# Performance work log

Hardware: AMD Instinct MI355X
Metric: run time of the kernel (lower is better)

The kernel has to match this reference:

```python
import jax, jax.numpy as jnp
import numpy as np
from jax import lax

B, C, H, W = 16, 384, 28, 28
HEADS = 8


def _ln(x, g, b):
    mu = jnp.mean(x, axis=-1, keepdims=True)
    var = jnp.var(x, axis=-1, keepdims=True)
    return (x - mu) * lax.rsqrt(var + 1e-5) * g + b


def setup_inputs() -> dict:
    key = jax.random.key(0)
    ks = jax.random.split(key, 8)
    s = 0.02
    return {
        "cls_token": jax.random.normal(ks[0], (B, 1, C), dtype=jnp.float32),
        "x": jax.random.normal(ks[1], (B, C, H, W), dtype=jnp.float32),
        "conv_w": jax.random.normal(ks[2], (C, 1, 3, 3), dtype=jnp.float32) * s,
        "conv_b": jnp.zeros((C,), jnp.float32),
        "ln1_g": jnp.ones((C,), jnp.float32),
        "ln1_b": jnp.zeros((C,), jnp.float32),
        "qkv_w": jax.random.normal(ks[3], (3 * C, C), dtype=jnp.float32) * s,
        "proj_w": jax.random.normal(ks[4], (C, C), dtype=jnp.float32) * s,
        "proj_b": jnp.zeros((C,), jnp.float32),
        "ln2_g": jnp.ones((C,), jnp.float32),
        "ln2_b": jnp.zeros((C,), jnp.float32),
        "fc1_w": jax.random.normal(ks[5], (4 * C, C), dtype=jnp.float32) * s,
        "fc1_b": jnp.zeros((4 * C,), jnp.float32),
        "fc2_w": jax.random.normal(ks[6], (C, 4 * C), dtype=jnp.float32) * s,
        "fc2_b": jnp.zeros((C,), jnp.float32),
    }


def reference(cls_token, x, conv_w, conv_b, ln1_g, ln1_b, qkv_w, proj_w, proj_b,
              ln2_g, ln2_b, fc1_w, fc1_b, fc2_w, fc2_b):
    Bv, Cv, Hv, Wv = x.shape
    h = HEADS
    d = Cv // h
    # depthwise 3x3 positional conv (groups=dim), residual add
    pe = lax.conv_general_dilated(
        x, conv_w, window_strides=(1, 1), padding="SAME",
        feature_group_count=Cv,
        dimension_numbers=("NCHW", "OIHW", "NCHW")) + conv_b[None, :, None, None]
    x = x + pe
    x_patch = x.reshape(Bv, Cv, Hv * Wv).transpose(0, 2, 1)  # [B, HW, C]
    xc = jnp.concatenate([cls_token, x_patch], axis=1)       # [B, N, C]
    N = xc.shape[1]

    # --- Attention with inline global_attn stats (first-call / int sentinel path) ---
    y = _ln(xc, ln1_g, ln1_b)
    qkv = (y @ qkv_w.T).reshape(Bv, N, 3, h, d)
    q = qkv[:, :, 0].transpose(0, 2, 1, 3)  # [B, h, N, d]
    k = qkv[:, :, 1].transpose(0, 2, 1, 3)
    v = qkv[:, :, 2].transpose(0, 2, 1, 3)
    scale = d ** -0.5
    attn = jax.nn.softmax(jnp.einsum("bhnd,bhmd->bhnm", q, k) * scale, axis=-1)
    # per-token global attention statistic: mean over heads of cls row (excl. cls)
    global_attn = jnp.mean(attn[:, :, 0, 1:], axis=1)  # [B, N-1]
    o = jnp.einsum("bhnm,bhmd->bhnd", attn, v).transpose(0, 2, 1, 3).reshape(Bv, N, Cv)
    xc = xc + (o @ proj_w.T + proj_b)

    # --- MLP (GELU exact, matching torch nn.GELU default) ---
    y2 = _ln(xc, ln2_g, ln2_b)
    m = jax.nn.gelu(y2 @ fc1_w.T + fc1_b, approximate=False) @ fc2_w.T + fc2_b
    xc = xc + m

    cls_out = xc[:, :1]                                            # [B, 1, C]
    x_out = xc[:, 1:].transpose(0, 2, 1).reshape(Bv, Cv, Hv, Wv)    # [B, C, H, W]
    return cls_out, x_out, global_attn
```

## Files before the change

### kernel.cpp

```cpp
#include <hip/hip_runtime.h>
#include <hip/hip_bf16.h>

#define DI __device__ __forceinline__

typedef __attribute__((ext_vector_type(4))) float f32x4;
typedef __attribute__((ext_vector_type(8))) short bf16x8;
typedef __attribute__((ext_vector_type(4))) short bf16x4;

static constexpr int CB = 16;
static constexpr int CC = 384;
static constexpr int CH = 28, CW = 28;
static constexpr int CD = 48;
static constexpr int CN = 785;
static constexpr int CM = CB * CN;
static constexpr int C3 = 3 * CC;
static constexpr int CF = 4 * CC;
static constexpr int HW = CH * CW;
static constexpr int NP = 832;

DI short f2b(float f) {
  __hip_bfloat16 h = __float2bfloat16(f);
  return *reinterpret_cast<short*>(&h);
}
DI float b2f(short s) {
  union { unsigned u; float f; } x;
  x.u = ((unsigned)(unsigned short)s) << 16;
  return x.f;
}

DI void gload16(const short* g, short* l) {
  __builtin_amdgcn_global_load_lds((const __attribute__((address_space(1))) void*)g,
                                   (__attribute__((address_space(3))) void*)l, 16, 0, 0);
}

__global__ void k_misc(const float* __restrict__ cls, float* __restrict__ xc,
                       float* __restrict__ ga) {
  const int gid = blockIdx.x * 256 + threadIdx.x;
  if (gid < CB * HW) ga[gid] = 0.f;
  if (gid < CB * CC) {
    const int b = gid / CC, c = gid % CC;
    xc[((size_t)b * CN) * CC + c] = cls[gid];
  }
}

__global__ void k_wconv(const float* __restrict__ s0, const float* __restrict__ s1,
                        const float* __restrict__ s2, const float* __restrict__ s3,
                        short* __restrict__ dst) {
  const int gid = (blockIdx.x * 256 + threadIdx.x) * 4;
  if (gid >= 1769472) return;
  const float* s; int off;
  if (gid < 442368)       { s = s0; off = gid; }
  else if (gid < 589824)  { s = s1; off = gid - 442368; }
  else if (gid < 1179648) { s = s2; off = gid - 589824; }
  else                    { s = s3; off = gid - 1179648; }
  f32x4 v = *(const f32x4*)(s + off);
  bf16x4 o;
#pragma unroll
  for (int i = 0; i < 4; i++) o[i] = f2b(v[i]);
  *(bf16x4*)(dst + gid) = o;
}

__global__ __launch_bounds__(256) void k_conv_t(const float* __restrict__ x,
                                                const float* __restrict__ cw,
                                                const float* __restrict__ cb,
                                                float* __restrict__ xc) {
  __shared__ float T[64][65];
  __shared__ float Wc[64 * 9];
  __shared__ float Cbs[64];
  const int b = blockIdx.z;
  const int cc = blockIdx.y * 64;
  const int hw0 = blockIdx.x * 64;
  const int t = threadIdx.x;
  const int hwi = t & 63, ci0 = t >> 6;
  const int hw = hw0 + hwi;
  const int yy = hw / CW, xx = hw % CW;
  const int ci2 = t & 63, hb2 = t >> 6;

  for (int i = t; i < 64 * 9; i += 256) Wc[i] = cw[cc * 9 + i];
  if (t < 64) Cbs[t] = cb[cc + t];
  __syncthreads();
  if (hw < HW) {
    const int ctr = yy * CW + xx;
    int off9[9]; float mk9[9];
#pragma unroll
    for (int ky = 0; ky < 3; ky++)
#pragma unroll
      for (int kx = 0; kx < 3; kx++) {
        const int iy = yy + ky - 1, ix = xx + kx - 1;
        const bool v = (iy >= 0 && iy < CH && ix >= 0 && ix < CW);
        off9[ky * 3 + kx] = v ? iy * CW + ix : ctr;
        mk9[ky * 3 + kx] = v ? 1.f : 0.f;
      }
#pragma unroll
    for (int j = 0; j < 16; j += 2) {
      const int cl0 = ci0 * 16 + j;
      const float* xp0 = x + ((size_t)(b * CC + cc + cl0)) * HW;
      const float* xp1 = xp0 + HW;
      float t0[9], t1[9];
#pragma unroll
      for (int q = 0; q < 9; q++) { t0[q] = xp0[off9[q]]; t1[q] = xp1[off9[q]]; }
      const float c0 = xp0[ctr], c1 = xp1[ctr];
      float a0 = Cbs[cl0], a1 = Cbs[cl0 + 1];
#pragma unroll
      for (int q = 0; q < 9; q++) {
        a0 += Wc[cl0 * 9 + q] * (t0[q] * mk9[q]);
        a1 += Wc[(cl0 + 1) * 9 + q] * (t1[q] * mk9[q]);
      }
      T[cl0][hwi] = c0 + a0;
      T[cl0 + 1][hwi] = c1 + a1;
    }
  }
  __syncthreads();
#pragma unroll
  for (int j = 0; j < 16; j++) {
    const int hwl = hb2 + j * 4;
    if (hw0 + hwl < HW)
      xc[((size_t)b * CN + 1 + hw0 + hwl) * CC + cc + ci2] = T[ci2][hwl];
  }
}

__global__ __launch_bounds__(256) void k_ln(const float* __restrict__ xin,
                                            const float* __restrict__ g,
                                            const float* __restrict__ bta,
                                            short* __restrict__ y, int Mtot) {
  const int row = blockIdx.x * 4 + (threadIdx.x >> 6);
  const int l = threadIdx.x & 63;
  if (row >= Mtot) return;
  const float* xr = xin + (size_t)row * CC;
  float v[6], s = 0.f, ss = 0.f;
#pragma unroll
  for (int i = 0; i < 6; i++) {
    v[i] = xr[l + i * 64];
    s += v[i];
    ss += v[i] * v[i];
  }
#pragma unroll
  for (int m = 1; m < 64; m <<= 1) { s += __shfl_xor(s, m); ss += __shfl_xor(ss, m); }
  const float mu = s * (1.f / CC);
  const float var = ss * (1.f / CC) - mu * mu;
  const float r = rsqrtf(var + 1e-5f);
#pragma unroll
  for (int i = 0; i < 6; i++) {
    const int c = l + i * 64;
    y[(size_t)row * CC + c] = f2b((v[i] - mu) * r * g[c] + bta[c]);
  }
}

template <int BM, int DOGELU, int DORES, int DOBIAS, int OUTBF>
__global__ __launch_bounds__(256) void k_gemm(const short* __restrict__ A,
                                              const short* __restrict__ W,
                                              const float* __restrict__ bias,
                                              const float* __restrict__ resid,
                                              void* __restrict__ out_,
                                              int M, int N, int K, int NN) {
  constexpr int MI = BM / 32;
  constexpr int ACALLS = BM / 64;
  constexpr int ASZ = BM * 32, BSZ = 128 * 32;
  __shared__ short As[2 * ASZ];
  __shared__ short Bs[2 * BSZ];

  const int nwg = gridDim.x;
  const int q = nwg >> 3, r = nwg & 7;
  const int x = blockIdx.x & 7, j = blockIdx.x >> 3;
  const int base = (x < r) ? x * (q + 1) : r * (q + 1) + (x - r) * q;
  const int wgid = base + j;
  const int bm = (wgid / NN) * BM, bn = (wgid % NN) * 128;

  const int t = threadIdx.x, w = t >> 6, l = t & 63, g = l >> 4, li = l & 15;
  const int wm = (w >> 1) * (BM / 2), wn = (w & 1) * 64;

  const int srow = l >> 2;
  const int scol = (l & 3) * 8;
  const short* aSrc[ACALLS]; int aOff[ACALLS];
#pragma unroll
  for (int jj = 0; jj < ACALLS; jj++) {
    int arow = bm + w * (BM / 4) + jj * 16 + srow; if (arow > M - 1) arow = M - 1;
    aSrc[jj] = A + (size_t)arow * K + scol;
    aOff[jj] = (w * (BM / 4) + jj * 16) * 32;
  }
  const short* bSrc[2]; int bOff[2];
#pragma unroll
  for (int jj = 0; jj < 2; jj++) {
    const int brow = bn + w * 32 + jj * 16 + srow;
    bSrc[jj] = W + (size_t)brow * K + scol;
    bOff[jj] = (w * 32 + jj * 16) * 32;
  }

  auto stage = [&](int buf, int kt) {
    const int ko = kt * 32;
#pragma unroll
    for (int jj = 0; jj < ACALLS; jj++)
      gload16(aSrc[jj] + ko, &As[buf * ASZ] + aOff[jj]);
#pragma unroll
    for (int jj = 0; jj < 2; jj++)
      gload16(bSrc[jj] + ko, &Bs[buf * BSZ] + bOff[jj]);
  };

  f32x4 acc[MI][4] = {};
  const int nkt = K / 32;
  stage(0, 0);
  __syncthreads();
  int cur = 0;
  for (int kt = 0; kt < nkt; kt++) {
    if (kt + 1 < nkt) stage(cur ^ 1, kt + 1);
    const short* Ab = &As[cur * ASZ];
    const short* Bb = &Bs[cur * BSZ];
    bf16x8 af[MI], bf[4];
#pragma unroll
    for (int mi = 0; mi < MI; mi++)
      af[mi] = *(const bf16x8*)&Ab[(wm + mi * 16 + li) * 32 + g * 8];
#pragma unroll
    for (int ni = 0; ni < 4; ni++)
      bf[ni] = *(const bf16x8*)&Bb[(wn + ni * 16 + li) * 32 + g * 8];
#pragma unroll
    for (int mi = 0; mi < MI; mi++)
#pragma unroll
      for (int ni = 0; ni < 4; ni++)
        acc[mi][ni] = __builtin_amdgcn_mfma_f32_16x16x32_bf16(af[mi], bf[ni], acc[mi][ni], 0, 0, 0);
    __syncthreads();
    cur ^= 1;
  }

#pragma unroll
  for (int mi = 0; mi < MI; mi++)
#pragma unroll
    for (int ni = 0; ni < 4; ni++) {
      const int col = bn + wn + ni * 16 + li;
      float bv = 0.f;
      if constexpr (DOBIAS) bv = bias[col];
#pragma unroll
      for (int rr = 0; rr < 4; rr++) {
        const int row = bm + wm + mi * 16 + g * 4 + rr;
        if (row < M) {
          float v = acc[mi][ni][rr] + bv;
          if constexpr (DOGELU) v = 0.5f * v * (1.f + erff(v * 0.7071067811865475f));
          if constexpr (DORES) v += resid[(size_t)row * N + col];
          if constexpr (OUTBF)
            ((short*)out_)[(size_t)row * N + col] = f2b(v);
          else
            ((float*)out_)[(size_t)row * N + col] = v;
        }
      }
    }
}

__global__ __launch_bounds__(256) void k_vt(const short* __restrict__ qkv,
                                            short* __restrict__ vt) {
  __shared__ short Tl[48 * 71];
  const int n0 = blockIdx.x * 64;
  const int bh = blockIdx.y;
  const int b = bh >> 3, h = bh & 7;
  const int t = threadIdx.x;
  const size_t bbase = (size_t)b * CN;
#pragma unroll
  for (int it = 0; it < 2; it++) {
    const int gi = t + it * 256;
    if (gi < 384) {
      const int nrel = gi / 6, dg = gi % 6;
      const int n = n0 + nrel;
      bf16x8 val = {};
      if (n < CN)
        val = *(const bf16x8*)(qkv + (bbase + n) * C3 + 2 * CC + h * CD + dg * 8);
#pragma unroll
      for (int i = 0; i < 8; i++) Tl[(dg * 8 + i) * 71 + nrel] = val[i];
    }
  }
  __syncthreads();
#pragma unroll
  for (int it = 0; it < 2; it++) {
    const int gj = t + it * 256;
    if (gj < 384) {
      const int d = gj >> 3, ng = gj & 7;
      bf16x8 v;
#pragma unroll
      for (int i = 0; i < 8; i++) v[i] = Tl[d * 71 + ng * 8 + i];
      *(bf16x8*)(vt + ((size_t)bh * CD + d) * NP + n0 + ng * 8) = v;
    }
  }
}

__global__ __launch_bounds__(256) void k_attn(const short* __restrict__ qkv,
                                              const short* __restrict__ vt,
                                              short* __restrict__ o) {
  __shared__ short Ks[64 * 48];
  __shared__ short Vs[48 * 64];
  const int f = blockIdx.x;
  const int xslot = f & 7, grp = f >> 3;
  const int bh = xslot + 8 * (grp & 15);
  const int qt = grp >> 4;
  const int b = bh >> 3, h = bh & 7;
  const int q0 = qt * 64;
  const int t = threadIdx.x, w = t >> 6, l = t & 63, g = l >> 4, li = l & 15;
  const size_t bbase = (size_t)b * CN;

  const int qrow = q0 + w * 16 + li;
  const int qr = qrow > CN - 1 ? CN - 1 : qrow;
  const short* qb = qkv + (bbase + qr) * C3 + h * CD;
  bf16x8 qf0 = *(const bf16x8*)(qb + g * 8);
  bf16x8 qf1 = {};
  if (g < 2) qf1 = *(const bf16x8*)(qb + 32 + g * 8);

  float mr = -1e30f, ls = 0.f;
  f32x4 oa[3] = {};
  const float scale = 0.14433756729740643f;

  const int krow0 = t / 6, kcg0 = t % 6;
  const int krow1 = (t + 256) / 6, kcg1 = (t + 256) % 6;
  const int vd0 = t >> 3, vkvg0 = t & 7;
  const int vd1 = (t + 256) >> 3, vkvg1 = (t + 256) & 7;
  const short* kbase = qkv + bbase * C3 + CC + h * CD;
  const short* vbase = vt + (size_t)bh * CD * NP;

  bf16x8 kr0 = {}, kr1 = {}, vr0 = {}, vr1 = {};
  kr0 = *(const bf16x8*)(kbase + (size_t)min(krow0, CN - 1) * C3 + kcg0 * 8);
  vr0 = *(const bf16x8*)(vbase + vd0 * NP + vkvg0 * 8);
  if (t < 128) {
    kr1 = *(const bf16x8*)(kbase + (size_t)min(krow1, CN - 1) * C3 + kcg1 * 8);
    vr1 = *(const bf16x8*)(vbase + vd1 * NP + vkvg1 * 8);
  }

  for (int kt = 0; kt < 13; kt++) {
    const int kv0 = kt * 64;
    __syncthreads();
    *(bf16x8*)((char*)Ks + ((krow0 * 96 + kcg0 * 16) ^ ((krow0 & 7) << 4))) = kr0;
    *(bf16x8*)((char*)Vs + ((vd0 * 128 + vkvg0 * 16) ^ ((vd0 & 7) << 4))) = vr0;
    if (t < 128) {
      *(bf16x8*)((char*)Ks + ((krow1 * 96 + kcg1 * 16) ^ ((krow1 & 7) << 4))) = kr1;
      *(bf16x8*)((char*)Vs + ((vd1 * 128 + vkvg1 * 16) ^ ((vd1 & 7) << 4))) = vr1;
    }
    __syncthreads();
    if (kt < 12) {
      const int kn = kv0 + 64;
      kr0 = *(const bf16x8*)(kbase + (size_t)min(kn + krow0, CN - 1) * C3 + kcg0 * 8);
      vr0 = *(const bf16x8*)(vbase + vd0 * NP + kn + vkvg0 * 8);
      if (t < 128) {
        kr1 = *(const bf16x8*)(kbase + (size_t)min(kn + krow1, CN - 1) * C3 + kcg1 * 8);
        vr1 = *(const bf16x8*)(vbase + vd1 * NP + kn + vkvg1 * 8);
      }
    }

    f32x4 s[4];
    __builtin_amdgcn_s_setprio(1);
#pragma unroll
    for (int ni = 0; ni < 4; ni++) {
      const int krw = ni * 16 + li;
      const int sw = (krw & 7) << 4;
      bf16x8 kf0 = *(const bf16x8*)((char*)Ks + ((krw * 96 + g * 16) ^ sw));
      bf16x8 kf1 = {};
      if (g < 2) kf1 = *(const bf16x8*)((char*)Ks + ((krw * 96 + 64 + g * 16) ^ sw));
      f32x4 acc = {};
      acc = __builtin_amdgcn_mfma_f32_16x16x32_bf16(kf0, qf0, acc, 0, 0, 0);
      acc = __builtin_amdgcn_mfma_f32_16x16x32_bf16(kf1, qf1, acc, 0, 0, 0);
      s[ni] = acc;
    }
    __builtin_amdgcn_s_setprio(0);

    float mt = -1e30f;
#pragma unroll
    for (int ni = 0; ni < 4; ni++)
#pragma unroll
      for (int rr = 0; rr < 4; rr++) {
        const int kva = kv0 + ni * 16 + g * 4 + rr;
        const float v = (kva < CN) ? s[ni][rr] * scale : -1e30f;
        s[ni][rr] = v;
        mt = fmaxf(mt, v);
      }
    mt = fmaxf(mt, __shfl_xor(mt, 16));
    mt = fmaxf(mt, __shfl_xor(mt, 32));
    const float mn = fmaxf(mr, mt);
    const float al = __expf(mr - mn);
    mr = mn;
    float ps = 0.f;
#pragma unroll
    for (int ni = 0; ni < 4; ni++)
#pragma unroll
      for (int rr = 0; rr < 4; rr++) {
        const float p = __expf(s[ni][rr] - mn);
        s[ni][rr] = p;
        ps += p;
      }
    ps += __shfl_xor(ps, 16);
    ps += __shfl_xor(ps, 32);
    ls = ls * al + ps;

    const int sb = (l & 48) + ((l & 48) >> 2);
    float ar[4];
#pragma unroll
    for (int rr = 0; rr < 4; rr++) ar[rr] = __shfl(al, sb + rr);
#pragma unroll
    for (int d = 0; d < 3; d++)
#pragma unroll
      for (int rr = 0; rr < 4; rr++) oa[d][rr] *= ar[rr];

    bf16x8 pa[2];
#pragma unroll
    for (int ks = 0; ks < 2; ks++)
#pragma unroll
      for (int i = 0; i < 8; i++)
        pa[ks][i] = f2b(i < 4 ? s[2 * ks][i] : s[2 * ks + 1][i - 4]);

    __builtin_amdgcn_s_setprio(1);
#pragma unroll
    for (int d = 0; d < 3; d++) {
      const int drow = d * 16 + li;
      const int sw = (drow & 7) << 4;
#pragma unroll
      for (int ks = 0; ks < 2; ks++) {
        bf16x4 lo = *(const bf16x4*)((char*)Vs + ((drow * 128 + ks * 64 + g * 8) ^ sw));
        bf16x4 hi = *(const bf16x4*)((char*)Vs + ((drow * 128 + ks * 64 + 32 + g * 8) ^ sw));
        bf16x8 vb;
#pragma unroll
        for (int i = 0; i < 4; i++) { vb[i] = lo[i]; vb[4 + i] = hi[i]; }
        oa[d] = __builtin_amdgcn_mfma_f32_16x16x32_bf16(pa[ks], vb, oa[d], 0, 0, 0);
      }
    }
    __builtin_amdgcn_s_setprio(0);
  }

  const int sb = (l & 48) + ((l & 48) >> 2);
  float lr[4];
#pragma unroll
  for (int rr = 0; rr < 4; rr++) lr[rr] = __shfl(ls, sb + rr);
#pragma unroll
  for (int d = 0; d < 3; d++)
#pragma unroll
    for (int rr = 0; rr < 4; rr++) {
      const int n = q0 + w * 16 + g * 4 + rr;
      if (n < CN)
        o[(bbase + n) * CC + h * CD + d * 16 + li] = f2b(oa[d][rr] / lr[rr]);
    }
}

__global__ __launch_bounds__(256) void k_gattn(const short* __restrict__ qkv,
                                               float* __restrict__ ga) {
  const int b = blockIdx.x >> 3, h = blockIdx.x & 7;
  __shared__ float red[4];
  const int t = threadIdx.x;
  const size_t bbase = (size_t)b * CN;
  const short* q0 = qkv + bbase * C3 + h * CD;
  float qv[CD];
#pragma unroll
  for (int i = 0; i < CD; i++) qv[i] = b2f(q0[i]);
  float lg[4], ev[4];
  float lmax = -1e30f;
#pragma unroll
  for (int j = 0; j < 4; j++) {
    const int m = t + j * 256;
    if (m < CN) {
      const short* kr = qkv + (bbase + m) * C3 + CC + h * CD;
      float acc = 0.f;
#pragma unroll
      for (int i = 0; i < CD; i++) acc += qv[i] * b2f(kr[i]);
      lg[j] = acc * 0.14433756729740643f;
      lmax = fmaxf(lmax, lg[j]);
    } else lg[j] = -1e30f;
  }
  for (int msk = 1; msk < 64; msk <<= 1) lmax = fmaxf(lmax, __shfl_xor(lmax, msk));
  if ((t & 63) == 0) red[t >> 6] = lmax;
  __syncthreads();
  lmax = fmaxf(fmaxf(red[0], red[1]), fmaxf(red[2], red[3]));
  __syncthreads();
  float es = 0.f;
#pragma unroll
  for (int j = 0; j < 4; j++) {
    ev[j] = (t + j * 256 < CN) ? __expf(lg[j] - lmax) : 0.f;
    es += ev[j];
  }
  for (int msk = 1; msk < 64; msk <<= 1) es += __shfl_xor(es, msk);
  if ((t & 63) == 0) red[t >> 6] = es;
  __syncthreads();
  es = red[0] + red[1] + red[2] + red[3];
  const float inv = 0.125f / es;
#pragma unroll
  for (int j = 0; j < 4; j++) {
    const int m = t + j * 256;
    if (m >= 1 && m < CN) atomicAdd(&ga[b * HW + m - 1], ev[j] * inv);
  }
}

__global__ __launch_bounds__(256) void k_out(const float* __restrict__ xc,
                                             float* __restrict__ outp) {
  const int b = blockIdx.y, tile = blockIdx.x, t = threadIdx.x;
  if (tile == 78) {
    for (int i = t; i < CC; i += 256)
      outp[b * CC + i] = xc[((size_t)b * CN) * CC + i];
    return;
  }
  __shared__ float T[64][65];
  const int ct = tile / 13, ht = tile % 13;
  const int c0 = ct * 64, hw0 = ht * 64;
  const int ci = t & 63, hb = t >> 6;
  for (int j = 0; j < 16; j++) {
    const int hwl = hb + j * 4;
    if (hw0 + hwl < HW)
      T[ci][hwl] = xc[((size_t)b * CN + 1 + hw0 + hwl) * CC + c0 + ci];
  }
  __syncthreads();
  const int hi = t & 63, cb2 = t >> 6;
  float* xo = outp + CB * CC;
  for (int j = 0; j < 16; j++) {
    const int cl = cb2 + j * 4;
    if (hw0 + hi < HW)
      xo[((size_t)(b * CC + c0 + cl)) * HW + hw0 + hi] = T[cl][hi];
  }
}

extern "C" void kernel_launch(void* const* d_in, const int* in_sizes, int n_in,
                              void* d_out, int out_size, void* d_ws, size_t ws_size,
                              hipStream_t stream) {
  const float* cls    = (const float*)d_in[0];
  const float* x      = (const float*)d_in[1];
  const float* conv_w = (const float*)d_in[2];
  const float* conv_b = (const float*)d_in[3];
  const float* ln1_g  = (const float*)d_in[4];
  const float* ln1_b  = (const float*)d_in[5];
  const float* qkv_w  = (const float*)d_in[6];
  const float* proj_w = (const float*)d_in[7];
  const float* proj_b = (const float*)d_in[8];
  const float* ln2_g  = (const float*)d_in[9];
  const float* ln2_b  = (const float*)d_in[10];
  const float* fc1_w  = (const float*)d_in[11];
  const float* fc1_b  = (const float*)d_in[12];
  const float* fc2_w  = (const float*)d_in[13];
  const float* fc2_b  = (const float*)d_in[14];

  float* outf = (float*)d_out;
  float* ga = outf + (size_t)CB * CC + (size_t)CB * CC * HW;
  short* vtb = (short*)(outf + CB * CC);

  char* ws = (char*)d_ws;
  float* xc   = (float*)ws;
  short* y    = (short*)(ws + 19292160ULL);
  short* qkvb = (short*)(ws + 28938240ULL);
  short* o    = (short*)(ws + 57876480ULL);
  short* m1   = (short*)(ws + 28938240ULL);
  short* wbuf = (short*)(ws + 67522560ULL);
  short* qkv_wb = wbuf;
  short* proj_wb = wbuf + 442368;
  short* fc1_wb  = wbuf + 589824;
  short* fc2_wb  = wbuf + 1179648;

  const int thr = 256;
  k_misc<<<49, thr, 0, stream>>>(cls, xc, ga);
  k_wconv<<<1728, thr, 0, stream>>>(qkv_w, proj_w, fc1_w, fc2_w, wbuf);
  k_conv_t<<<dim3(13, 6, CB), thr, 0, stream>>>(x, conv_w, conv_b, xc);
  k_ln<<<CM / 4, thr, 0, stream>>>(xc, ln1_g, ln1_b, y, CM);
  k_gemm<128, 0, 0, 0, 1><<<99 * 9, thr, 0, stream>>>(
      y, qkv_wb, nullptr, nullptr, qkvb, CM, C3, CC, 9);
  k_vt<<<dim3(13, CB * 8), thr, 0, stream>>>(qkvb, vtb);
  k_attn<<<1664, thr, 0, stream>>>(qkvb, vtb, o);
  k_gattn<<<CB * 8, thr, 0, stream>>>(qkvb, ga);
  k_gemm<64, 0, 1, 1, 0><<<197 * 3, thr, 0, stream>>>(
      o, proj_wb, proj_b, xc, xc, CM, CC, CC, 3);
  k_ln<<<CM / 4, thr, 0, stream>>>(xc, ln2_g, ln2_b, y, CM);
  k_gemm<128, 1, 0, 1, 1><<<99 * 12, thr, 0, stream>>>(
      y, fc1_wb, fc1_b, nullptr, m1, CM, CF, CC, 12);
  k_gemm<64, 0, 1, 1, 0><<<197 * 3, thr, 0, stream>>>(
      m1, fc2_wb, fc2_b, xc, xc, CM, CC, CF, 3);
  k_out<<<dim3(79, CB), thr, 0, stream>>>(xc, outf);
}
```

Before: 325.9 us.

## Double-buffer attention K/V tiles and add lazy softmax rescaling with exp2

Result: slower. 336.2 us (+3.1%).

```diff
diff --git a/kernel.cpp b/kernel.cpp
--- a/kernel.cpp
+++ b/kernel.cpp
@@ -282,8 +282,8 @@
 __global__ __launch_bounds__(256) void k_attn(const short* __restrict__ qkv,
                                               const short* __restrict__ vt,
                                               short* __restrict__ o) {
-  __shared__ short Ks[64 * 48];
-  __shared__ short Vs[48 * 64];
+  __shared__ short Ks[2][64 * 48];
+  __shared__ short Vs[2][48 * 64];
   const int f = blockIdx.x;
   const int xslot = f & 7, grp = f >> 3;
   const int bh = xslot + 8 * (grp & 15);
@@ -293,61 +293,92 @@
   const int t = threadIdx.x, w = t >> 6, l = t & 63, g = l >> 4, li = l & 15;
   const size_t bbase = (size_t)b * CN;
 
+  const float SC = 0.14433756729740643f * 1.4426950408889634f;
   const int qrow = q0 + w * 16 + li;
   const int qr = qrow > CN - 1 ? CN - 1 : qrow;
   const short* qb = qkv + (bbase + qr) * C3 + h * CD;
-  bf16x8 qf0 = *(const bf16x8*)(qb + g * 8);
-  bf16x8 qf1 = {};
-  if (g < 2) qf1 = *(const bf16x8*)(qb + 32 + g * 8);
+  bf16x8 qf0, qf1 = {};
+  {
+    bf16x8 q0r = *(const bf16x8*)(qb + g * 8);
+#pragma unroll
+    for (int i = 0; i < 8; i++) qf0[i] = f2b(b2f(q0r[i]) * SC);
+    if (g < 2) {
+      bf16x8 q1r = *(const bf16x8*)(qb + 32 + g * 8);
+#pragma unroll
+      for (int i = 0; i < 8; i++) qf1[i] = f2b(b2f(q1r[i]) * SC);
+    }
+  }
 
   float mr = -1e30f, ls = 0.f;
   f32x4 oa[3] = {};
-  const float scale = 0.14433756729740643f;
 
   const int krow0 = t / 6, kcg0 = t % 6;
   const int krow1 = (t + 256) / 6, kcg1 = (t + 256) % 6;
   const int vd0 = t >> 3, vkvg0 = t & 7;
   const int vd1 = (t + 256) >> 3, vkvg1 = (t + 256) & 7;
+  const int ksb0 = (krow0 * 96 + kcg0 * 16) ^ ((krow0 & 7) << 4);
+  const int ksb1 = (krow1 * 96 + kcg1 * 16) ^ ((krow1 & 7) << 4);
+  const int vsb0 = (vd0 * 128 + vkvg0 * 16) ^ ((vd0 & 7) << 4);
+  const int vsb1 = (vd1 * 128 + vkvg1 * 16) ^ ((vd1 & 7) << 4);
   const short* kbase = qkv + bbase * C3 + CC + h * CD;
   const short* vbase = vt + (size_t)bh * CD * NP;
-
-  bf16x8 kr0 = {}, kr1 = {}, vr0 = {}, vr1 = {};
-  kr0 = *(const bf16x8*)(kbase + (size_t)min(krow0, CN - 1) * C3 + kcg0 * 8);
-  vr0 = *(const bf16x8*)(vbase + vd0 * NP + vkvg0 * 8);
+  const short* kp0 = kbase + (size_t)krow0 * C3 + kcg0 * 8;
+  const short* kp1 = kbase + (size_t)krow1 * C3 + kcg1 * 8;
+  const short* vp0 = vbase + vd0 * NP + vkvg0 * 8;
+  const short* vp1 = vbase + vd1 * NP + vkvg1 * 8;
+
+  bf16x8 kr0, kr1 = {}, vr0, vr1 = {};
+  kr0 = *(const bf16x8*)kp0;  vr0 = *(const bf16x8*)vp0;
+  if (t < 128) { kr1 = *(const bf16x8*)kp1; vr1 = *(const bf16x8*)vp1; }
+  *(bf16x8*)((char*)Ks[0] + ksb0) = kr0;
+  *(bf16x8*)((char*)Vs[0] + vsb0) = vr0;
   if (t < 128) {
-    kr1 = *(const bf16x8*)(kbase + (size_t)min(krow1, CN - 1) * C3 + kcg1 * 8);
-    vr1 = *(const bf16x8*)(vbase + vd1 * NP + vkvg1 * 8);
-  }
+    *(bf16x8*)((char*)Ks[0] + ksb1) = kr1;
+    *(bf16x8*)((char*)Vs[0] + vsb1) = vr1;
+  }
+  kp0 += 64 * C3; vp0 += 64; kp1 += 64 * C3; vp1 += 64;
+  kr0 = *(const bf16x8*)kp0;  vr0 = *(const bf16x8*)vp0;
+  if (t < 128) { kr1 = *(const bf16x8*)kp1; vr1 = *(const bf16x8*)vp1; }
+  __syncthreads();
 
   for (int kt = 0; kt < 13; kt++) {
-    const int kv0 = kt * 64;
-    __syncthreads();
-    *(bf16x8*)((char*)Ks + ((krow0 * 96 + kcg0 * 16) ^ ((krow0 & 7) << 4))) = kr0;
-    *(bf16x8*)((char*)Vs + ((vd0 * 128 + vkvg0 * 16) ^ ((vd0 & 7) << 4))) = vr0;
-    if (t < 128) {
-      *(bf16x8*)((char*)Ks + ((krow1 * 96 + kcg1 * 16) ^ ((krow1 & 7) << 4))) = kr1;
-      *(bf16x8*)((char*)Vs + ((vd1 * 128 + vkvg1 * 16) ^ ((vd1 & 7) << 4))) = vr1;
-    }
-    __syncthreads();
+    const int cur = kt & 1, nxt = cur ^ 1;
     if (kt < 12) {
-      const int kn = kv0 + 64;
-      kr0 = *(const bf16x8*)(kbase + (size_t)min(kn + krow0, CN - 1) * C3 + kcg0 * 8);
-      vr0 = *(const bf16x8*)(vbase + vd0 * NP + kn + vkvg0 * 8);
+      *(bf16x8*)((char*)Ks[nxt] + ksb0) = kr0;
+      *(bf16x8*)((char*)Vs[nxt] + vsb0) = vr0;
       if (t < 128) {
-        kr1 = *(const bf16x8*)(kbase + (size_t)min(kn + krow1, CN - 1) * C3 + kcg1 * 8);
-        vr1 = *(const bf16x8*)(vbase + vd1 * NP + kn + vkvg1 * 8);
+        *(bf16x8*)((char*)Ks[nxt] + ksb1) = kr1;
+        *(bf16x8*)((char*)Vs[nxt] + vsb1) = vr1;
       }
     }
-
+    if (kt + 2 <= 12) {
+      kp0 += 64 * C3; vp0 += 64; kp1 += 64 * C3; vp1 += 64;
+      if (kt + 2 < 12) {
+        kr0 = *(const bf16x8*)kp0; vr0 = *(const bf16x8*)vp0;
+        if (t < 128) { kr1 = *(const bf16x8*)kp1; vr1 = *(const bf16x8*)vp1; }
+      } else {
+        const short* kq0 = (768 + krow0 <= CN - 1) ? kp0
+                          : kbase + (size_t)(CN - 1) * C3 + kcg0 * 8;
+        kr0 = *(const bf16x8*)kq0; vr0 = *(const bf16x8*)vp0;
+        if (t < 128) {
+          const short* kq1 = (768 + krow1 <= CN - 1) ? kp1
+                            : kbase + (size_t)(CN - 1) * C3 + kcg1 * 8;
+          kr1 = *(const bf16x8*)kq1; vr1 = *(const bf16x8*)vp1;
+        }
+      }
+    }
+
+    const char* KsC = (const char*)Ks[cur];
+    const char* VsC = (const char*)Vs[cur];
     f32x4 s[4];
     __builtin_amdgcn_s_setprio(1);
 #pragma unroll
     for (int ni = 0; ni < 4; ni++) {
       const int krw = ni * 16 + li;
       const int sw = (krw & 7) << 4;
-      bf16x8 kf0 = *(const bf16x8*)((char*)Ks + ((krw * 96 + g * 16) ^ sw));
+      bf16x8 kf0 = *(const bf16x8*)(KsC + ((krw * 96 + g * 16) ^ sw));
       bf16x8 kf1 = {};
-      if (g < 2) kf1 = *(const bf16x8*)((char*)Ks + ((krw * 96 + 64 + g * 16) ^ sw));
+      if (g < 2) kf1 = *(const bf16x8*)(KsC + ((krw * 96 + 64 + g * 16) ^ sw));
       f32x4 acc = {};
       acc = __builtin_amdgcn_mfma_f32_16x16x32_bf16(kf0, qf0, acc, 0, 0, 0);
       acc = __builtin_amdgcn_mfma_f32_16x16x32_bf16(kf1, qf1, acc, 0, 0, 0);
@@ -355,42 +386,49 @@
     }
     __builtin_amdgcn_s_setprio(0);
 
-    float mt = -1e30f;
+    if (kt == 12) {
+#pragma unroll
+      for (int ni = 0; ni < 4; ni++)
+#pragma unroll
+        for (int rr = 0; rr < 4; rr++)
+          if (768 + ni * 16 + g * 4 + rr >= CN) s[ni][rr] = -1e30f;
+    }
+
+    float mt = s[0][0];
 #pragma unroll
     for (int ni = 0; ni < 4; ni++)
 #pragma unroll
-      for (int rr = 0; rr < 4; rr++) {
-        const int kva = kv0 + ni * 16 + g * 4 + rr;
-        const float v = (kva < CN) ? s[ni][rr] * scale : -1e30f;
-        s[ni][rr] = v;
-        mt = fmaxf(mt, v);
-      }
+      for (int rr = 0; rr < 4; rr++) mt = fmaxf(mt, s[ni][rr]);
     mt = fmaxf(mt, __shfl_xor(mt, 16));
     mt = fmaxf(mt, __shfl_xor(mt, 32));
-    const float mn = fmaxf(mr, mt);
-    const float al = __expf(mr - mn);
-    mr = mn;
+
+    if (!__all(mt - mr <= 8.f)) {
+      const float mn = fmaxf(mr, mt);
+      const float al = __builtin_exp2f(mr - mn);
+      mr = mn;
+      ls *= al;
+      const int sb = (l & 48) + ((l & 48) >> 2);
+      float ar[4];
+#pragma unroll
+      for (int rr = 0; rr < 4; rr++) ar[rr] = __shfl(al, sb + rr);
+#pragma unroll
+      for (int d = 0; d < 3; d++)
+#pragma unroll
+        for (int rr = 0; rr < 4; rr++) oa[d][rr] *= ar[rr];
+    }
+
     float ps = 0.f;
 #pragma unroll
     for (int ni = 0; ni < 4; ni++)
 #pragma unroll
       for (int rr = 0; rr < 4; rr++) {
-        const float p = __expf(s[ni][rr] - mn);
+        const float p = __builtin_exp2f(s[ni][rr] - mr);
         s[ni][rr] = p;
         ps += p;
       }
     ps += __shfl_xor(ps, 16);
     ps += __shfl_xor(ps, 32);
-    ls = ls * al + ps;
-
-    const int sb = (l & 48) + ((l & 48) >> 2);
-    float ar[4];
-#pragma unroll
-    for (int rr = 0; rr < 4; rr++) ar[rr] = __shfl(al, sb + rr);
-#pragma unroll
-    for (int d = 0; d < 3; d++)
-#pragma unroll
-      for (int rr = 0; rr < 4; rr++) oa[d][rr] *= ar[rr];
+    ls += ps;
 
     bf16x8 pa[2];
 #pragma unroll
@@ -406,8 +444,8 @@
       const int sw = (drow & 7) << 4;
 #pragma unroll
       for (int ks = 0; ks < 2; ks++) {
-        bf16x4 lo = *(const bf16x4*)((char*)Vs + ((drow * 128 + ks * 64 + g * 8) ^ sw));
-        bf16x4 hi = *(const bf16x4*)((char*)Vs + ((drow * 128 + ks * 64 + 32 + g * 8) ^ sw));
+        bf16x4 lo = *(const bf16x4*)(VsC + ((drow * 128 + ks * 64 + g * 8) ^ sw));
+        bf16x4 hi = *(const bf16x4*)(VsC + ((drow * 128 + ks * 64 + 32 + g * 8) ^ sw));
         bf16x8 vb;
 #pragma unroll
         for (int i = 0; i < 4; i++) { vb[i] = lo[i]; vb[4 + i] = hi[i]; }
@@ -415,6 +453,10 @@
       }
     }
     __builtin_amdgcn_s_setprio(0);
+
+    asm volatile("s_waitcnt lgkmcnt(0)" ::: "memory");
+    __builtin_amdgcn_sched_barrier(0);
+    __builtin_amdgcn_s_barrier();
   }
 
   const int sb = (l & 48) + ((l & 48) >> 2);
```

## Fold softmax scale into Q, use exp2, lazy rescale, merge misc kernel

Applied to the files above, without the earlier changes.

Result: slower. 334.8 us (+2.7%).

```diff
diff --git a/kernel.cpp b/kernel.cpp
--- a/kernel.cpp
+++ b/kernel.cpp
@@ -33,20 +33,18 @@
                                    (__attribute__((address_space(3))) void*)l, 16, 0, 0);
 }
 
-__global__ void k_misc(const float* __restrict__ cls, float* __restrict__ xc,
-                       float* __restrict__ ga) {
-  const int gid = blockIdx.x * 256 + threadIdx.x;
-  if (gid < CB * HW) ga[gid] = 0.f;
-  if (gid < CB * CC) {
-    const int b = gid / CC, c = gid % CC;
-    xc[((size_t)b * CN) * CC + c] = cls[gid];
-  }
-}
-
 __global__ void k_wconv(const float* __restrict__ s0, const float* __restrict__ s1,
                         const float* __restrict__ s2, const float* __restrict__ s3,
-                        short* __restrict__ dst) {
-  const int gid = (blockIdx.x * 256 + threadIdx.x) * 4;
+                        short* __restrict__ dst,
+                        const float* __restrict__ cls, float* __restrict__ xc,
+                        float* __restrict__ ga) {
+  const int gid0 = blockIdx.x * 256 + threadIdx.x;
+  if (gid0 < CB * HW) ga[gid0] = 0.f;
+  if (gid0 < CB * CC) {
+    const int b = gid0 / CC, c = gid0 % CC;
+    xc[((size_t)b * CN) * CC + c] = cls[gid0];
+  }
+  const int gid = gid0 * 4;
   if (gid >= 1769472) return;
   const float* s; int off;
   if (gid < 442368)       { s = s0; off = gid; }
@@ -293,16 +291,24 @@
   const int t = threadIdx.x, w = t >> 6, l = t & 63, g = l >> 4, li = l & 15;
   const size_t bbase = (size_t)b * CN;
 
+  const float SC = 0.14433756729740643f * 1.4426950408889634f;
   const int qrow = q0 + w * 16 + li;
   const int qr = qrow > CN - 1 ? CN - 1 : qrow;
   const short* qb = qkv + (bbase + qr) * C3 + h * CD;
-  bf16x8 qf0 = *(const bf16x8*)(qb + g * 8);
-  bf16x8 qf1 = {};
-  if (g < 2) qf1 = *(const bf16x8*)(qb + 32 + g * 8);
+  bf16x8 qf0, qf1 = {};
+  {
+    bf16x8 q0r = *(const bf16x8*)(qb + g * 8);
+#pragma unroll
+    for (int i = 0; i < 8; i++) qf0[i] = f2b(b2f(q0r[i]) * SC);
+    if (g < 2) {
+      bf16x8 q1r = *(const bf16x8*)(qb + 32 + g * 8);
+#pragma unroll
+      for (int i = 0; i < 8; i++) qf1[i] = f2b(b2f(q1r[i]) * SC);
+    }
+  }
 
   float mr = -1e30f, ls = 0.f;
   f32x4 oa[3] = {};
-  const float scale = 0.14433756729740643f;
 
   const int krow0 = t / 6, kcg0 = t % 6;
   const int krow1 = (t + 256) / 6, kcg1 = (t + 256) % 6;
@@ -355,42 +361,49 @@
     }
     __builtin_amdgcn_s_setprio(0);
 
-    float mt = -1e30f;
+    if (kt == 12) {
+#pragma unroll
+      for (int ni = 0; ni < 4; ni++)
+#pragma unroll
+        for (int rr = 0; rr < 4; rr++)
+          if (768 + ni * 16 + g * 4 + rr >= CN) s[ni][rr] = -1e30f;
+    }
+
+    float mt = s[0][0];
 #pragma unroll
     for (int ni = 0; ni < 4; ni++)
 #pragma unroll
-      for (int rr = 0; rr < 4; rr++) {
-        const int kva = kv0 + ni * 16 + g * 4 + rr;
-        const float v = (kva < CN) ? s[ni][rr] * scale : -1e30f;
-        s[ni][rr] = v;
-        mt = fmaxf(mt, v);
-      }
+      for (int rr = 0; rr < 4; rr++) mt = fmaxf(mt, s[ni][rr]);
     mt = fmaxf(mt, __shfl_xor(mt, 16));
     mt = fmaxf(mt, __shfl_xor(mt, 32));
-    const float mn = fmaxf(mr, mt);
-    const float al = __expf(mr - mn);
-    mr = mn;
+
+    if (!__all(mt - mr <= 8.f)) {
+      const float mn = fmaxf(mr, mt);
+      const float al = __builtin_exp2f(mr - mn);
+      mr = mn;
+      ls *= al;
+      const int sb = (l & 48) + ((l & 48) >> 2);
+      float ar[4];
+#pragma unroll
+      for (int rr = 0; rr < 4; rr++) ar[rr] = __shfl(al, sb + rr);
+#pragma unroll
+      for (int d = 0; d < 3; d++)
+#pragma unroll
+        for (int rr = 0; rr < 4; rr++) oa[d][rr] *= ar[rr];
+    }
+
     float ps = 0.f;
 #pragma unroll
     for (int ni = 0; ni < 4; ni++)
 #pragma unroll
       for (int rr = 0; rr < 4; rr++) {
-        const float p = __expf(s[ni][rr] - mn);
+        const float p = __builtin_exp2f(s[ni][rr] - mr);
         s[ni][rr] = p;
         ps += p;
       }
     ps += __shfl_xor(ps, 16);
     ps += __shfl_xor(ps, 32);
-    ls = ls * al + ps;
-
-    const int sb = (l & 48) + ((l & 48) >> 2);
-    float ar[4];
-#pragma unroll
-    for (int rr = 0; rr < 4; rr++) ar[rr] = __shfl(al, sb + rr);
-#pragma unroll
-    for (int d = 0; d < 3; d++)
-#pragma unroll
-      for (int rr = 0; rr < 4; rr++) oa[d][rr] *= ar[rr];
+    ls += ps;
 
     bf16x8 pa[2];
 #pragma unroll
@@ -541,8 +554,7 @@
   short* fc2_wb  = wbuf + 1179648;
 
   const int thr = 256;
-  k_misc<<<49, thr, 0, stream>>>(cls, xc, ga);
-  k_wconv<<<1728, thr, 0, stream>>>(qkv_w, proj_w, fc1_w, fc2_w, wbuf);
+  k_wconv<<<1728, thr, 0, stream>>>(qkv_w, proj_w, fc1_w, fc2_w, wbuf, cls, xc, ga);
   k_conv_t<<<dim3(13, 6, CB), thr, 0, stream>>>(x, conv_w, conv_b, xc);
   k_ln<<<CM / 4, thr, 0, stream>>>(xc, ln1_g, ln1_b, y, CM);
   k_gemm<128, 0, 0, 0, 1><<<99 * 9, thr, 0, stream>>>(
```
